# Performance work log

Measured on AMD Instinct MI355X. Metric: run time of the kernel, lower is better.

Reference implementation:

```python
import jax, jax.numpy as jnp
import numpy as np

B, N, K = 4, 4096, 16
DP, DM = 128, 512


def _gather(points, idx):
    # points [B,N,C], idx [B,N,K] -> [B,N,K,C] (index_points)
    b, n, k = idx.shape
    flat = jnp.take_along_axis(points, idx.reshape(b, -1)[:, :, None], axis=1)
    return flat.reshape(b, n, k, points.shape[-1])


def _mlp2(x, w1, b1, w2, b2):
    return jax.nn.relu(x @ w1 + b1) @ w2 + b2


def setup_inputs():
    key = jax.random.key(0)
    ks = jax.random.split(key, 20)
    s_dp = 1.0 / np.sqrt(DP)
    s_dm = 1.0 / np.sqrt(DM)
    return {
        "xyz": jax.random.normal(ks[0], (B, N, 3), jnp.float32),
        "features": jax.random.normal(ks[1], (B, N, DP), jnp.float32),
        "fc1_w": jax.random.normal(ks[2], (DP, DM), jnp.float32) * s_dp,
        "fc1_b": jnp.zeros((DM,), jnp.float32),
        "fc2_w": jax.random.normal(ks[3], (DM, DP), jnp.float32) * s_dm,
        "fc2_b": jnp.zeros((DP,), jnp.float32),
        "wq": jax.random.normal(ks[4], (DM, DM), jnp.float32) * s_dm,
        "wk": jax.random.normal(ks[5], (DM, DM), jnp.float32) * s_dm,
        "wv": jax.random.normal(ks[6], (DM, DM), jnp.float32) * s_dm,
        "d1_w": jax.random.normal(ks[7], (3, DM), jnp.float32) * (1.0 / np.sqrt(3.0)),
        "d1_b": jnp.zeros((DM,), jnp.float32),
        "d2_w": jax.random.normal(ks[8], (DM, DM), jnp.float32) * s_dm,
        "d2_b": jnp.zeros((DM,), jnp.float32),
        "g1_w": jax.random.normal(ks[9], (DM, DM), jnp.float32) * s_dm,
        "g1_b": jnp.zeros((DM,), jnp.float32),
        "g2_w": jax.random.normal(ks[10], (DM, DM), jnp.float32) * s_dm,
        "g2_b": jnp.zeros((DM,), jnp.float32),
    }


def reference(xyz, features, fc1_w, fc1_b, fc2_w, fc2_b, wq, wk, wv,
              d1_w, d1_b, d2_w, d2_b, g1_w, g1_b, g2_w, g2_b):
    # square_distance via ||a-b||^2 = |a|^2 + |b|^2 - 2 a.b  (avoids [B,N,N,3])
    sq = jnp.sum(xyz * xyz, axis=-1)                       # [B,N]
    dists = sq[:, :, None] + sq[:, None, :] - 2.0 * jnp.einsum('bnc,bmc->bnm', xyz, xyz)
    knn_idx = jax.lax.top_k(-dists, K)[1]                  # [B,N,K] k-nearest
    knn_xyz = _gather(xyz, knn_idx)                        # [B,N,K,3]

    pre = features
    x = features @ fc1_w + fc1_b                           # [B,N,DM]
    q = x @ wq                                             # [B,N,DM]
    k = _gather(x @ wk, knn_idx)                           # [B,N,K,DM]
    v = _gather(x @ wv, knn_idx)                           # [B,N,K,DM]

    pos_enc = _mlp2(xyz[:, :, None] - knn_xyz, d1_w, d1_b, d2_w, d2_b)  # [B,N,K,DM]
    attn = _mlp2(q[:, :, None] - k + pos_enc, g1_w, g1_b, g2_w, g2_b)   # [B,N,K,DM]
    attn = jax.nn.softmax(attn / np.sqrt(DM), axis=-2)     # softmax over neighbors
    res = jnp.sum(attn * (v + pos_enc), axis=2)            # einsum bmnf,bmnf->bmf
    res = res @ fc2_w + fc2_b + pre                        # [B,N,DP]
    return res, attn
```

## Files before the change

### kernel.cpp

```cpp
#include <hip/hip_runtime.h>

#define NPTS   4096
#define NBATCH 4
#define KNN    16
#define DMODEL 512
#define DPOINT 128
#define QKVLD  1536

#define BM 128
#define BN 128
#define BK 64

typedef unsigned short bfu;
typedef __attribute__((ext_vector_type(8))) short short8;
typedef __attribute__((ext_vector_type(4))) float f32x4;

__device__ __forceinline__ bfu f2bf(float f) {
    unsigned u = __builtin_bit_cast(unsigned, f);
    return (bfu)((u + 0x7fffu + ((u >> 16) & 1u)) >> 16);
}
__device__ __forceinline__ float bf2f(bfu h) {
    unsigned u = ((unsigned)h) << 16;
    return __builtin_bit_cast(float, u);
}

__device__ __forceinline__ void gload_lds16(const bfu* g, bfu* l) {
    __builtin_amdgcn_global_load_lds(
        (const __attribute__((address_space(1))) void*)g,
        (__attribute__((address_space(3))) void*)l, 16, 0, 0);
}

#define TPQ 8
#define QPB 32

__device__ __forceinline__ void knn_merge_level(float* bd, int* bi, int lvl)
{
    float pd[KNN]; int pi[KNN];
#pragma unroll
    for (int i = 0; i < KNN; ++i) {
        pd[i] = __shfl_xor(bd[KNN-1-i], lvl);
        pi[i] = __shfl_xor(bi[KNN-1-i], lvl);
    }
#pragma unroll
    for (int i = 0; i < KNN; ++i) {
        bool take = (pd[i] < bd[i]) || (pd[i] == bd[i] && pi[i] < bi[i]);
        if (take) { bd[i] = pd[i]; bi[i] = pi[i]; }
    }
#pragma unroll
    for (int s = 8; s >= 1; s >>= 1) {
#pragma unroll
        for (int i = 0; i < KNN; ++i) {
            if ((i & s) == 0) {
                const int j = i + s;
                bool sw = (bd[j] < bd[i]) || (bd[j] == bd[i] && bi[j] < bi[i]);
                if (sw) {
                    float td = bd[i]; bd[i] = bd[j]; bd[j] = td;
                    int   ti = bi[i]; bi[i] = bi[j]; bi[j] = ti;
                }
            }
        }
    }
}

__global__ __launch_bounds__(256) void knn_kernel(const float* __restrict__ xyz,
                                                  int* __restrict__ knn_out)
{
    __shared__ float4 pts[NPTS];
    const int b    = blockIdx.y;
    const int tid  = threadIdx.x;
    const int qloc = tid >> 3;
    const int sub  = tid & 7;
    const int n    = blockIdx.x * QPB + qloc;

    const float* bx = xyz + (size_t)b * NPTS * 3;
    for (int i = tid; i < NPTS; i += 256) {
        float x = bx[i*3+0], y = bx[i*3+1], z = bx[i*3+2];
        pts[i] = make_float4(x, y, z, x*x + y*y + z*z);
    }
    __syncthreads();

    const float4 me = pts[n];
    float bd[KNN];
    int   bi[KNN];
#pragma unroll
    for (int i = 0; i < KNN; ++i) { bd[i] = 3.4e38f; bi[i] = -1; }

    for (int t0 = 0; t0 < NPTS / TPQ; t0 += 8) {
        float d[8];
#pragma unroll
        for (int j = 0; j < 8; ++j) {
            float4 o = pts[sub + ((t0 + j) << 3)];
            d[j] = me.w + o.w - 2.f*(me.x*o.x + me.y*o.y + me.z*o.z);
        }
        float mn = fminf(fminf(fminf(d[0],d[1]),fminf(d[2],d[3])),
                         fminf(fminf(d[4],d[5]),fminf(d[6],d[7])));
        if (mn < bd[KNN-1]) {
#pragma unroll
            for (int j = 0; j < 8; ++j) {
                float dj = d[j];
                if (dj < bd[KNN-1]) {
                    const int m = sub + ((t0 + j) << 3);
#pragma unroll
                    for (int i = KNN-1; i >= 1; --i) {
                        float dp = bd[i-1];
                        if (dp > dj)        { bd[i] = dp; bi[i] = bi[i-1]; }
                        else if (bd[i] > dj){ bd[i] = dj; bi[i] = m; }
                    }
                    if (bd[0] > dj) { bd[0] = dj; bi[0] = m; }
                }
            }
        }
    }

    knn_merge_level(bd, bi, 1);
    knn_merge_level(bd, bi, 2);
    knn_merge_level(bd, bi, 4);

    int* orow = knn_out + ((size_t)b*NPTS + n) * KNN;
    const int base = b * NPTS;
    orow[sub*2+0] = base + bi[sub*2+0];
    orow[sub*2+1] = base + bi[sub*2+1];
}

__global__ __launch_bounds__(256) void cvt_bf16(const float* __restrict__ src,
                                                bfu* __restrict__ dst, int n4)
{
    int i = blockIdx.x * 256 + threadIdx.x;
    if (i < n4) {
        float4 v = ((const float4*)src)[i];
        bfu* d = dst + (size_t)i * 4;
        d[0] = f2bf(v.x); d[1] = f2bf(v.y); d[2] = f2bf(v.z); d[3] = f2bf(v.w);
    }
}

__global__ __launch_bounds__(256) void transpose_cvt(const float* __restrict__ src,
                                                     bfu* __restrict__ dst,
                                                     int K, int N)
{
    int i = blockIdx.x * 256 + threadIdx.x;
    if (i < K * N) {
        int n = i / K, k = i - n * K;
        dst[i] = f2bf(src[(size_t)k * N + n]);
    }
}

template<int ASRC, bool BIAS, bool RELU, bool OUTBF, bool RESID, bool SMAX>
__global__ __launch_bounds__(256) void gemm_mfma(
    const bfu* __restrict__ A, const bfu* __restrict__ BT,
    const float* __restrict__ bias, const float* __restrict__ resid,
    void* __restrict__ Cout, int M, int Kd, int Nd,
    const float* __restrict__ xyz, const int* __restrict__ knng,
    const float* __restrict__ d1w, const float* __restrict__ d1b,
    const bfu* __restrict__ qb, const bfu* __restrict__ kb,
    const bfu* __restrict__ posc, const bfu* __restrict__ vb,
    bfu* __restrict__ resbuf, int row_base)
{
    __shared__ bfu As[BM * BK];
    __shared__ bfu Bs[BN * BK];

    const int tid  = threadIdx.x;
    const int lane = tid & 63;
    const int w    = tid >> 6;
    const int bm   = blockIdx.x * BM;
    const int bn   = blockIdx.y * BN;
    const int wm   = (w >> 1) * 64;
    const int wn   = (w & 1) * 64;
    const int lrow = lane & 15;
    const int kgrp = lane >> 4;

    f32x4 acc[4][4];
#pragma unroll
    for (int m = 0; m < 4; ++m)
#pragma unroll
        for (int n = 0; n < 4; ++n) acc[m][n] = (f32x4){0.f, 0.f, 0.f, 0.f};

    int   grow = 0, gnb = 0;
    float rx = 0.f, ry = 0.f, rz = 0.f;
    if constexpr (ASRC != 0) {
        int r = tid >> 1;
        grow  = row_base + bm + r;
        gnb   = knng[grow];
        if constexpr (ASRC == 1) {
            int p = grow >> 4;
            rx = xyz[(size_t)p*3+0] - xyz[(size_t)gnb*3+0];
            ry = xyz[(size_t)p*3+1] - xyz[(size_t)gnb*3+1];
            rz = xyz[(size_t)p*3+2] - xyz[(size_t)gnb*3+2];
        }
    }

    __shared__ float d1s[(ASRC == 1) ? 4 * DMODEL : 1];
    if constexpr (ASRC == 1) {
        for (int i = tid; i < DMODEL; i += 256) d1s[i] = d1b[i];
        for (int i = tid; i < 3 * DMODEL; i += 256) d1s[DMODEL + i] = d1w[i];
    }

    for (int k0 = 0; k0 < Kd; k0 += BK) {
        __syncthreads();

        {
            int r0 = w * 32;
            const bfu* gB = BT + (size_t)(bn + r0 + (lane >> 3)) * Kd + k0 + (lane & 7) * 8;
            bfu* lB = Bs + r0 * BK;
#pragma unroll
            for (int i = 0; i < 4; ++i)
                gload_lds16(gB + (size_t)i * 8 * Kd, lB + i * 8 * BK);
        }

        if constexpr (ASRC == 0) {
            int r0 = w * 32;
            const bfu* gA = A + (size_t)(bm + r0 + (lane >> 3)) * Kd + k0 + (lane & 7) * 8;
            bfu* lA = As + r0 * BK;
#pragma unroll
            for (int i = 0; i < 4; ++i)
                gload_lds16(gA + (size_t)i * 8 * Kd, lA + i * 8 * BK);
        } else if constexpr (ASRC == 1) {
            int r = tid >> 1, cseg = (tid & 1) * 32;
#pragma unroll
            for (int c8 = 0; c8 < 4; ++c8) {
                short8 ov;
#pragma unroll
                for (int h = 0; h < 2; ++h) {
                    int kk2 = k0 + cseg + c8 * 8 + h * 4;
                    float4 fb = *(const float4*)&d1s[kk2];
                    float4 fx = *(const float4*)&d1s[DMODEL   + kk2];
                    float4 fy = *(const float4*)&d1s[2*DMODEL + kk2];
                    float4 fz = *(const float4*)&d1s[3*DMODEL + kk2];
                    ov[h*4+0] = (short)f2bf(fmaxf(fmaf(rz,fz.x,fmaf(ry,fy.x,fmaf(rx,fx.x,fb.x))),0.f));
                    ov[h*4+1] = (short)f2bf(fmaxf(fmaf(rz,fz.y,fmaf(ry,fy.y,fmaf(rx,fx.y,fb.y))),0.f));
                    ov[h*4+2] = (short)f2bf(fmaxf(fmaf(rz,fz.z,fmaf(ry,fy.z,fmaf(rx,fx.z,fb.z))),0.f));
                    ov[h*4+3] = (short)f2bf(fmaxf(fmaf(rz,fz.w,fmaf(ry,fy.w,fmaf(rx,fx.w,fb.w))),0.f));
                }
                *(short8*)&As[r * BK + cseg + c8 * 8] = ov;
            }
        } else {
            int r = tid >> 1, cseg = (tid & 1) * 32;
            int p = grow >> 4;
            const bfu* qrow = qb   + (size_t)p    * QKVLD + k0 + cseg;
            const bfu* krow = kb   + (size_t)gnb  * QKVLD + k0 + cseg;
            const bfu* prow = posc + (size_t)(bm + r) * DMODEL + k0 + cseg;
#pragma unroll
            for (int c8 = 0; c8 < 4; ++c8) {
                short8 qv = *(const short8*)(qrow + c8 * 8);
                short8 kv = *(const short8*)(krow + c8 * 8);
                short8 pv = *(const short8*)(prow + c8 * 8);
                short8 ov;
#pragma unroll
                for (int j = 0; j < 8; ++j) {
                    float v = bf2f((bfu)qv[j]) - bf2f((bfu)kv[j]) + bf2f((bfu)pv[j]);
                    ov[j] = (short)f2bf(v);
                }
                *(short8*)&As[r * BK + cseg + c8 * 8] = ov;
            }
        }

        __syncthreads();

#pragma unroll
        for (int kk = 0; kk < BK; kk += 32) {
            short8 af[4], bfr[4];
#pragma unroll
            for (int m = 0; m < 4; ++m)
                af[m] = *(const short8*)&As[(wm + m * 16 + lrow) * BK + kk + kgrp * 8];
#pragma unroll
            for (int n = 0; n < 4; ++n)
                bfr[n] = *(const short8*)&Bs[(wn + n * 16 + lrow) * BK + kk + kgrp * 8];
#pragma unroll
            for (int m = 0; m < 4; ++m)
#pragma unroll
                for (int n = 0; n < 4; ++n)
                    acc[m][n] = __builtin_amdgcn_mfma_f32_16x16x32_bf16(
                        af[m], bfr[n], acc[m][n], 0, 0, 0);
        }
    }

    if constexpr (SMAX) {
        const float scale = 0.044194173824159216f;
#pragma unroll
        for (int m = 0; m < 4; ++m) {
            const int row0 = bm + wm + m * 16 + kgrp * 4;
            const int ploc = (bm + wm + m * 16) >> 4;
            int gnb4[4];
#pragma unroll
            for (int r = 0; r < 4; ++r) gnb4[r] = knng[(size_t)row_base + row0 + r];
#pragma unroll
            for (int n = 0; n < 4; ++n) {
                const int col = bn + wn + n * 16 + lrow;
                const float bv = bias[col];
                float v0 = (acc[m][n][0] + bv) * scale;
                float v1 = (acc[m][n][1] + bv) * scale;
                float v2 = (acc[m][n][2] + bv) * scale;
                float v3 = (acc[m][n][3] + bv) * scale;
                float mx = fmaxf(fmaxf(v0, v1), fmaxf(v2, v3));
                mx = fmaxf(mx, __shfl_xor(mx, 16));
                mx = fmaxf(mx, __shfl_xor(mx, 32));
                float e0 = __expf(v0 - mx), e1 = __expf(v1 - mx);
                float e2 = __expf(v2 - mx), e3 = __expf(v3 - mx);
                float s = e0 + e1 + e2 + e3;
                s += __shfl_xor(s, 16);
                s += __shfl_xor(s, 32);
                const float inv = 1.f / s;
                float a0 = e0*inv, a1 = e1*inv, a2 = e2*inv, a3 = e3*inv;
                float* ao = (float*)Cout;
                ao[(size_t)(row0 + 0) * DMODEL + col] = a0;
                ao[(size_t)(row0 + 1) * DMODEL + col] = a1;
                ao[(size_t)(row0 + 2) * DMODEL + col] = a2;
                ao[(size_t)(row0 + 3) * DMODEL + col] = a3;
                float res = 0.f;
                res = fmaf(a0, bf2f(vb[(size_t)gnb4[0]*QKVLD + col]) + bf2f(posc[(size_t)(row0+0)*DMODEL + col]), res);
                res = fmaf(a1, bf2f(vb[(size_t)gnb4[1]*QKVLD + col]) + bf2f(posc[(size_t)(row0+1)*DMODEL + col]), res);
                res = fmaf(a2, bf2f(vb[(size_t)gnb4[2]*QKVLD + col]) + bf2f(posc[(size_t)(row0+2)*DMODEL + col]), res);
                res = fmaf(a3, bf2f(vb[(size_t)gnb4[3]*QKVLD + col]) + bf2f(posc[(size_t)(row0+3)*DMODEL + col]), res);
                res += __shfl_xor(res, 16);
                res += __shfl_xor(res, 32);
                if (kgrp == 0) {
                    const size_t pglob = (size_t)(row_base >> 4) + ploc;
                    resbuf[pglob * DMODEL + col] = f2bf(res);
                }
            }
        }
        return;
    }

#pragma unroll
    for (int m = 0; m < 4; ++m) {
#pragma unroll
        for (int n = 0; n < 4; ++n) {
            int col = bn + wn + n * 16 + lrow;
            float bv = BIAS ? bias[col] : 0.f;
#pragma unroll
            for (int r = 0; r < 4; ++r) {
                int row = bm + wm + m * 16 + kgrp * 4 + r;
                float v = acc[m][n][r] + bv;
                if (RESID) v += resid[(size_t)row * Nd + col];
                if (RELU)  v = fmaxf(v, 0.f);
                if (OUTBF) ((bfu*)Cout)[(size_t)row * Nd + col] = f2bf(v);
                else     ((float*)Cout)[(size_t)row * Nd + col] = v;
            }
        }
    }
}

extern "C" void kernel_launch(void* const* d_in, const int* in_sizes, int n_in,
                              void* d_out, int out_size, void* d_ws, size_t ws_size,
                              hipStream_t stream)
{
    const float* xyz      = (const float*)d_in[0];
    const float* features = (const float*)d_in[1];
    const float* fc1_w    = (const float*)d_in[2];
    const float* fc1_b    = (const float*)d_in[3];
    const float* fc2_w    = (const float*)d_in[4];
    const float* fc2_b    = (const float*)d_in[5];
    const float* wq       = (const float*)d_in[6];
    const float* wk       = (const float*)d_in[7];
    const float* wv       = (const float*)d_in[8];
    const float* d1_w     = (const float*)d_in[9];
    const float* d1_b     = (const float*)d_in[10];
    const float* d2_w     = (const float*)d_in[11];
    const float* d2_b     = (const float*)d_in[12];
    const float* g1_w     = (const float*)d_in[13];
    const float* g1_b     = (const float*)d_in[14];
    const float* g2_w     = (const float*)d_in[15];
    const float* g2_b     = (const float*)d_in[16];

    const size_t Mpts  = (size_t)NBATCH * NPTS;
    const size_t Mrows = Mpts * KNN;
    float* out_res  = (float*)d_out;
    float* out_attn = (float*)d_out + Mpts * DPOINT;

    size_t off = 0;
    auto ab = [&](size_t elems) { bfu* r = (bfu*)((char*)d_ws + off); off += elems * 2; return r; };
    bfu* fc1T  = ab((size_t)DMODEL * DPOINT);
    bfu* qkvT  = ab((size_t)QKVLD * DMODEL);
    bfu* d2T   = ab((size_t)DMODEL * DMODEL);
    bfu* g1T   = ab((size_t)DMODEL * DMODEL);
    bfu* g2T   = ab((size_t)DMODEL * DMODEL);
    bfu* fc2T  = ab((size_t)DPOINT * DMODEL);
    bfu* featb = ab(Mpts * DPOINT);
    bfu* xb    = ab(Mpts * DMODEL);
    bfu* qkvb  = ab(Mpts * QKVLD);
    bfu* resb  = ab(Mpts * DMODEL);
    int* knng  = (int*)((char*)d_ws + off); off += Mrows * 4;

    int nchunk = 32;
    {
        const int cands[6] = {1, 2, 4, 8, 16, 32};
        for (int i = 0; i < 6; ++i) {
            size_t need = off + 2ull * (Mrows / cands[i]) * DMODEL * 2;
            if (need <= ws_size) { nchunk = cands[i]; break; }
        }
    }
    const size_t Rc  = Mrows / nchunk;
    bfu* posc = ab(Rc * DMODEL);
    bfu* hc   = ab(Rc * DMODEL);

    knn_kernel<<<dim3(NPTS/QPB, NBATCH), 256, 0, stream>>>(xyz, knng);

    transpose_cvt<<<dim3((DPOINT*DMODEL+255)/256), 256, 0, stream>>>(fc1_w, fc1T, DPOINT, DMODEL);
    transpose_cvt<<<dim3((DMODEL*DMODEL+255)/256), 256, 0, stream>>>(wq, qkvT,                 DMODEL, DMODEL);
    transpose_cvt<<<dim3((DMODEL*DMODEL+255)/256), 256, 0, stream>>>(wk, qkvT +   DMODEL*DMODEL, DMODEL, DMODEL);
    transpose_cvt<<<dim3((DMODEL*DMODEL+255)/256), 256, 0, stream>>>(wv, qkvT + 2*DMODEL*DMODEL, DMODEL, DMODEL);
    transpose_cvt<<<dim3((DMODEL*DMODEL+255)/256), 256, 0, stream>>>(d2_w, d2T, DMODEL, DMODEL);
    transpose_cvt<<<dim3((DMODEL*DMODEL+255)/256), 256, 0, stream>>>(g1_w, g1T, DMODEL, DMODEL);
    transpose_cvt<<<dim3((DMODEL*DMODEL+255)/256), 256, 0, stream>>>(g2_w, g2T, DMODEL, DMODEL);
    transpose_cvt<<<dim3((DMODEL*DPOINT+255)/256), 256, 0, stream>>>(fc2_w, fc2T, DMODEL, DPOINT);
    cvt_bf16<<<dim3((Mpts*DPOINT/4+255)/256), 256, 0, stream>>>(features, featb, (int)(Mpts*DPOINT/4));

#define GEMM_ARGS(Ap, Bp, biasp, residp, Cp, M_, K_, N_, rb) \
    (Ap), (Bp), (biasp), (residp), (Cp), (int)(M_), (int)(K_), (int)(N_), \
    xyz, knng, d1_w, d1_b, qkvb, qkvb + DMODEL, posc, qkvb + 2*DMODEL, resb, (int)(rb)

    gemm_mfma<0, true,  false, true,  false, false><<<dim3(Mpts/BM, DMODEL/BN), 256, 0, stream>>>(
        GEMM_ARGS(featb, fc1T, fc1_b, nullptr, xb, Mpts, DPOINT, DMODEL, 0));
    gemm_mfma<0, false, false, true,  false, false><<<dim3(Mpts/BM, QKVLD/BN), 256, 0, stream>>>(
        GEMM_ARGS(xb, qkvT, nullptr, nullptr, qkvb, Mpts, DMODEL, QKVLD, 0));

    for (int c = 0; c < nchunk; ++c) {
        const size_t rb = (size_t)c * Rc;
        float* attn_c = out_attn + rb * DMODEL;

        gemm_mfma<1, true, false, true, false, false><<<dim3(Rc/BM, DMODEL/BN), 256, 0, stream>>>(
            GEMM_ARGS(nullptr, d2T, d2_b, nullptr, posc, Rc, DMODEL, DMODEL, rb));
        gemm_mfma<2, true, true,  true, false, false><<<dim3(Rc/BM, DMODEL/BN), 256, 0, stream>>>(
            GEMM_ARGS(nullptr, g1T, g1_b, nullptr, hc, Rc, DMODEL, DMODEL, rb));
        gemm_mfma<0, false, false, false, false, true><<<dim3(Rc/BM, DMODEL/BN), 256, 0, stream>>>(
            GEMM_ARGS(hc, g2T, g2_b, nullptr, attn_c, Rc, DMODEL, DMODEL, rb));
    }

    gemm_mfma<0, true, false, false, true, false><<<dim3(Mpts/BM, DPOINT/BN), 256, 0, stream>>>(
        GEMM_ARGS(resb, fc2T, fc2_b, features, out_res, Mpts, DMODEL, DPOINT, 0));
#undef GEMM_ARGS
}
```

Measured before the change: 2.121 ms.

## Precompute pos-encoding hidden layer separately and template GEMM row tile size

The first positional MLP layer (3->512 with relu) moves out of the d2 GEMM's A-tile loader into a standalone elementwise kernel. That kernel writes bf16 activations into the hc buffer, and the d2 GEMM then reads them as a plain bf16 A operand through the direct global-to-LDS path. The GEMM row tile size becomes a template parameter, and small chunks use a 64-row tile so more workgroups are launched. resb now aliases xb, which saves workspace and may allow fewer chunks. The cost is an extra kernel launch and a write plus read of the hidden activations per chunk.

```diff
diff --git a/kernel.cpp b/kernel.cpp
--- a/kernel.cpp
+++ b/kernel.cpp
@@ -7,7 +7,6 @@
 #define DPOINT 128
 #define QKVLD  1536
 
-#define BM 128
 #define BN 128
 #define BK 64
 
@@ -144,54 +143,71 @@
     }
 }
 
-template<int ASRC, bool BIAS, bool RELU, bool OUTBF, bool RESID, bool SMAX>
+__global__ __launch_bounds__(256) void pos_h_kernel(
+    const float* __restrict__ xyz, const int* __restrict__ knng,
+    const float* __restrict__ d1w, const float* __restrict__ d1b,
+    bfu* __restrict__ out, int row_base)
+{
+    const int idx  = blockIdx.x * 256 + threadIdx.x;
+    const int rloc = idx >> 6;
+    const int c0   = (idx & 63) * 8;
+    const int grow = row_base + rloc;
+    const int p    = grow >> 4;
+    const int nb   = knng[grow];
+    const float rx = xyz[(size_t)p*3+0] - xyz[(size_t)nb*3+0];
+    const float ry = xyz[(size_t)p*3+1] - xyz[(size_t)nb*3+1];
+    const float rz = xyz[(size_t)p*3+2] - xyz[(size_t)nb*3+2];
+    short8 ov;
+#pragma unroll
+    for (int j = 0; j < 8; ++j) {
+        const int k = c0 + j;
+        float v = d1b[k];
+        v = fmaf(rx, d1w[k],        v);
+        v = fmaf(ry, d1w[512 + k],  v);
+        v = fmaf(rz, d1w[1024 + k], v);
+        ov[j] = (short)f2bf(fmaxf(v, 0.f));
+    }
+    *(short8*)&out[(size_t)rloc * DMODEL + c0] = ov;
+}
+
+template<int BMt, int ASRC, bool BIAS, bool RELU, bool OUTBF, bool RESID, bool SMAX>
 __global__ __launch_bounds__(256) void gemm_mfma(
     const bfu* __restrict__ A, const bfu* __restrict__ BT,
     const float* __restrict__ bias, const float* __restrict__ resid,
     void* __restrict__ Cout, int M, int Kd, int Nd,
-    const float* __restrict__ xyz, const int* __restrict__ knng,
-    const float* __restrict__ d1w, const float* __restrict__ d1b,
+    const int* __restrict__ knng,
     const bfu* __restrict__ qb, const bfu* __restrict__ kb,
     const bfu* __restrict__ posc, const bfu* __restrict__ vb,
     bfu* __restrict__ resbuf, int row_base)
 {
-    __shared__ bfu As[BM * BK];
+    constexpr int MF  = BMt / 32;
+    constexpr int TPR = 256 / BMt;
+    constexpr int RPW = BMt / 4;
+
+    __shared__ bfu As[BMt * BK];
     __shared__ bfu Bs[BN * BK];
 
     const int tid  = threadIdx.x;
     const int lane = tid & 63;
     const int w    = tid >> 6;
-    const int bm   = blockIdx.x * BM;
+    const int bm   = blockIdx.x * BMt;
     const int bn   = blockIdx.y * BN;
-    const int wm   = (w >> 1) * 64;
+    const int wm   = (w >> 1) * (BMt / 2);
     const int wn   = (w & 1) * 64;
     const int lrow = lane & 15;
     const int kgrp = lane >> 4;
 
-    f32x4 acc[4][4];
-#pragma unroll
-    for (int m = 0; m < 4; ++m)
+    f32x4 acc[MF][4];
+#pragma unroll
+    for (int m = 0; m < MF; ++m)
 #pragma unroll
         for (int n = 0; n < 4; ++n) acc[m][n] = (f32x4){0.f, 0.f, 0.f, 0.f};
 
-    int   grow = 0, gnb = 0;
-    float rx = 0.f, ry = 0.f, rz = 0.f;
-    if constexpr (ASRC != 0) {
-        int r = tid >> 1;
+    int grow = 0, gnb = 0;
+    if constexpr (ASRC == 2) {
+        int r = tid / TPR;
         grow  = row_base + bm + r;
         gnb   = knng[grow];
-        if constexpr (ASRC == 1) {
-            int p = grow >> 4;
-            rx = xyz[(size_t)p*3+0] - xyz[(size_t)gnb*3+0];
-            ry = xyz[(size_t)p*3+1] - xyz[(size_t)gnb*3+1];
-            rz = xyz[(size_t)p*3+2] - xyz[(size_t)gnb*3+2];
-        }
-    }
-
-    __shared__ float d1s[(ASRC == 1) ? 4 * DMODEL : 1];
-    if constexpr (ASRC == 1) {
-        for (int i = tid; i < DMODEL; i += 256) d1s[i] = d1b[i];
-        for (int i = tid; i < 3 * DMODEL; i += 256) d1s[DMODEL + i] = d1w[i];
     }
 
     for (int k0 = 0; k0 < Kd; k0 += BK) {
@@ -207,39 +223,21 @@
         }
 
         if constexpr (ASRC == 0) {
-            int r0 = w * 32;
+            int r0 = w * RPW;
             const bfu* gA = A + (size_t)(bm + r0 + (lane >> 3)) * Kd + k0 + (lane & 7) * 8;
             bfu* lA = As + r0 * BK;
 #pragma unroll
-            for (int i = 0; i < 4; ++i)
+            for (int i = 0; i < RPW / 8; ++i)
                 gload_lds16(gA + (size_t)i * 8 * Kd, lA + i * 8 * BK);
-        } else if constexpr (ASRC == 1) {
-            int r = tid >> 1, cseg = (tid & 1) * 32;
-#pragma unroll
-            for (int c8 = 0; c8 < 4; ++c8) {
-                short8 ov;
-#pragma unroll
-                for (int h = 0; h < 2; ++h) {
-                    int kk2 = k0 + cseg + c8 * 8 + h * 4;
-                    float4 fb = *(const float4*)&d1s[kk2];
-                    float4 fx = *(const float4*)&d1s[DMODEL   + kk2];
-                    float4 fy = *(const float4*)&d1s[2*DMODEL + kk2];
-                    float4 fz = *(const float4*)&d1s[3*DMODEL + kk2];
-                    ov[h*4+0] = (short)f2bf(fmaxf(fmaf(rz,fz.x,fmaf(ry,fy.x,fmaf(rx,fx.x,fb.x))),0.f));
-                    ov[h*4+1] = (short)f2bf(fmaxf(fmaf(rz,fz.y,fmaf(ry,fy.y,fmaf(rx,fx.y,fb.y))),0.f));
-                    ov[h*4+2] = (short)f2bf(fmaxf(fmaf(rz,fz.z,fmaf(ry,fy.z,fmaf(rx,fx.z,fb.z))),0.f));
-                    ov[h*4+3] = (short)f2bf(fmaxf(fmaf(rz,fz.w,fmaf(ry,fy.w,fmaf(rx,fx.w,fb.w))),0.f));
-                }
-                *(short8*)&As[r * BK + cseg + c8 * 8] = ov;
-            }
         } else {
-            int r = tid >> 1, cseg = (tid & 1) * 32;
+            constexpr int NC8 = (BK / TPR) / 8;
+            int r = tid / TPR, cseg = (tid % TPR) * (BK / TPR);
             int p = grow >> 4;
             const bfu* qrow = qb   + (size_t)p    * QKVLD + k0 + cseg;
             const bfu* krow = kb   + (size_t)gnb  * QKVLD + k0 + cseg;
             const bfu* prow = posc + (size_t)(bm + r) * DMODEL + k0 + cseg;
 #pragma unroll
-            for (int c8 = 0; c8 < 4; ++c8) {
+            for (int c8 = 0; c8 < NC8; ++c8) {
                 short8 qv = *(const short8*)(qrow + c8 * 8);
                 short8 kv = *(const short8*)(krow + c8 * 8);
                 short8 pv = *(const short8*)(prow + c8 * 8);
@@ -257,15 +255,15 @@
 
 #pragma unroll
         for (int kk = 0; kk < BK; kk += 32) {
-            short8 af[4], bfr[4];
-#pragma unroll
-            for (int m = 0; m < 4; ++m)
+            short8 af[MF], bfr[4];
+#pragma unroll
+            for (int m = 0; m < MF; ++m)
                 af[m] = *(const short8*)&As[(wm + m * 16 + lrow) * BK + kk + kgrp * 8];
 #pragma unroll
             for (int n = 0; n < 4; ++n)
                 bfr[n] = *(const short8*)&Bs[(wn + n * 16 + lrow) * BK + kk + kgrp * 8];
 #pragma unroll
-            for (int m = 0; m < 4; ++m)
+            for (int m = 0; m < MF; ++m)
 #pragma unroll
                 for (int n = 0; n < 4; ++n)
                     acc[m][n] = __builtin_amdgcn_mfma_f32_16x16x32_bf16(
@@ -276,7 +274,7 @@
     if constexpr (SMAX) {
         const float scale = 0.044194173824159216f;
 #pragma unroll
-        for (int m = 0; m < 4; ++m) {
+        for (int m = 0; m < MF; ++m) {
             const int row0 = bm + wm + m * 16 + kgrp * 4;
             const int ploc = (bm + wm + m * 16) >> 4;
             int gnb4[4];
@@ -322,7 +320,7 @@
     }
 
 #pragma unroll
-    for (int m = 0; m < 4; ++m) {
+    for (int m = 0; m < MF; ++m) {
 #pragma unroll
         for (int n = 0; n < 4; ++n) {
             int col = bn + wn + n * 16 + lrow;
@@ -378,7 +376,7 @@
     bfu* featb = ab(Mpts * DPOINT);
     bfu* xb    = ab(Mpts * DMODEL);
     bfu* qkvb  = ab(Mpts * QKVLD);
-    bfu* resb  = ab(Mpts * DMODEL);
+    bfu* resb  = xb;
     int* knng  = (int*)((char*)d_ws + off); off += Mrows * 4;
 
     int nchunk = 32;
@@ -405,28 +403,35 @@
     transpose_cvt<<<dim3((DMODEL*DPOINT+255)/256), 256, 0, stream>>>(fc2_w, fc2T, DMODEL, DPOINT);
     cvt_bf16<<<dim3((Mpts*DPOINT/4+255)/256), 256, 0, stream>>>(features, featb, (int)(Mpts*DPOINT/4));
 
-#define GEMM_ARGS(Ap, Bp, biasp, residp, Cp, M_, K_, N_, rb) \
+#define GARGS(Ap, Bp, biasp, residp, Cp, M_, K_, N_, rb) \
     (Ap), (Bp), (biasp), (residp), (Cp), (int)(M_), (int)(K_), (int)(N_), \
-    xyz, knng, d1_w, d1_b, qkvb, qkvb + DMODEL, posc, qkvb + 2*DMODEL, resb, (int)(rb)
-
-    gemm_mfma<0, true,  false, true,  false, false><<<dim3(Mpts/BM, DMODEL/BN), 256, 0, stream>>>(
-        GEMM_ARGS(featb, fc1T, fc1_b, nullptr, xb, Mpts, DPOINT, DMODEL, 0));
-    gemm_mfma<0, false, false, true,  false, false><<<dim3(Mpts/BM, QKVLD/BN), 256, 0, stream>>>(
-        GEMM_ARGS(xb, qkvT, nullptr, nullptr, qkvb, Mpts, DMODEL, QKVLD, 0));
+    knng, qkvb, qkvb + DMODEL, posc, qkvb + 2*DMODEL, resb, (int)(rb)
+
+    gemm_mfma<128, 0, true,  false, true,  false, false><<<dim3(Mpts/128, DMODEL/BN), 256, 0, stream>>>(
+        GARGS(featb, fc1T, fc1_b, nullptr, xb, Mpts, DPOINT, DMODEL, 0));
+    gemm_mfma<128, 0, false, false, true,  false, false><<<dim3(Mpts/128, QKVLD/BN), 256, 0, stream>>>(
+        GARGS(xb, qkvT, nullptr, nullptr, qkvb, Mpts, DMODEL, QKVLD, 0));
 
     for (int c = 0; c < nchunk; ++c) {
         const size_t rb = (size_t)c * Rc;
         float* attn_c = out_attn + rb * DMODEL;
 
-        gemm_mfma<1, true, false, true, false, false><<<dim3(Rc/BM, DMODEL/BN), 256, 0, stream>>>(
-            GEMM_ARGS(nullptr, d2T, d2_b, nullptr, posc, Rc, DMODEL, DMODEL, rb));
-        gemm_mfma<2, true, true,  true, false, false><<<dim3(Rc/BM, DMODEL/BN), 256, 0, stream>>>(
-            GEMM_ARGS(nullptr, g1T, g1_b, nullptr, hc, Rc, DMODEL, DMODEL, rb));
-        gemm_mfma<0, false, false, false, false, true><<<dim3(Rc/BM, DMODEL/BN), 256, 0, stream>>>(
-            GEMM_ARGS(hc, g2T, g2_b, nullptr, attn_c, Rc, DMODEL, DMODEL, rb));
-    }
-
-    gemm_mfma<0, true, false, false, true, false><<<dim3(Mpts/BM, DPOINT/BN), 256, 0, stream>>>(
-        GEMM_ARGS(resb, fc2T, fc2_b, features, out_res, Mpts, DMODEL, DPOINT, 0));
-#undef GEMM_ARGS
-}
+        pos_h_kernel<<<dim3((unsigned)(Rc/4)), 256, 0, stream>>>(xyz, knng, d1_w, d1_b, hc, (int)rb);
+
+#define CHUNK_LAUNCH(BMT) \
+        gemm_mfma<BMT, 0, true, false, true, false, false><<<dim3(Rc/BMT, DMODEL/BN), 256, 0, stream>>>( \
+            GARGS(hc, d2T, d2_b, nullptr, posc, Rc, DMODEL, DMODEL, rb)); \
+        gemm_mfma<BMT, 2, true, true,  true, false, false><<<dim3(Rc/BMT, DMODEL/BN), 256, 0, stream>>>( \
+            GARGS(nullptr, g1T, g1_b, nullptr, hc, Rc, DMODEL, DMODEL, rb)); \
+        gemm_mfma<BMT, 0, false, false, false, false, true><<<dim3(Rc/BMT, DMODEL/BN), 256, 0, stream>>>( \
+            GARGS(hc, g2T, g2_b, nullptr, attn_c, Rc, DMODEL, DMODEL, rb));
+
+        if (Rc >= 32768) { CHUNK_LAUNCH(128) }
+        else             { CHUNK_LAUNCH(64)  }
+#undef CHUNK_LAUNCH
+    }
+
+    gemm_mfma<128, 0, true, false, false, true, false><<<dim3(Mpts/128, DPOINT/BN), 256, 0, stream>>>(
+        GARGS(resb, fc2T, fc2_b, features, out_res, Mpts, DMODEL, DPOINT, 0));
+#undef GARGS
+}
```

New measurement: 2.195 ms. 3.5% more time.
